# Optimization experiments

Hardware: AMD Instinct MI355X
Metric: run time of the kernel (lower is better)

## Reference

```python
import jax, jax.numpy as jnp
import numpy as np
import math

H = 16
SEG = 128
DIL = 2


def hilbert_perm(M: int) -> jnp.ndarray:
    # Boustrophedon (snake) traversal of a ceil(sqrt(M)) grid, matching
    # create_hilbert_mapping_simple: skip linear positions >= M, keep first M.
    g = int(math.ceil(math.sqrt(M)))
    grid = np.arange(g * g).reshape(g, g)
    grid[1::2] = grid[1::2, ::-1]
    flat = grid.reshape(-1)
    flat = flat[flat < M][:M]
    return jnp.asarray(flat, dtype=jnp.int32)


def setup_inputs() -> dict:
    key = jax.random.key(0)
    kx, kq, ko = jax.random.split(key, 3)
    B, M, D = 4, 4096, 1024
    x = jax.random.normal(kx, (B, M, D), dtype=jnp.float32)
    # nn.Linear weights: [out_features, in_features], y = x @ W.T
    w_qkv = jax.random.normal(kq, (3 * D, D), dtype=jnp.float32) * (D ** -0.5)
    w_out = jax.random.normal(ko, (D, D), dtype=jnp.float32) * (D ** -0.5)
    return {"x": x, "w_qkv": w_qkv, "w_out": w_out}


def reference(x, w_qkv, w_out):
    B, M, Dm = x.shape
    hd = Dm // H
    scale = hd ** -0.5
    S = M // SEG  # number of segments (M chosen as a multiple of SEG)

    qkv = x @ w_qkv.T                              # [B, M, 3*Dm]
    qkv = qkv.reshape(B, M, 3, H, hd)
    q = qkv[:, :, 0].transpose(0, 2, 1, 3)         # [B, H, M, hd]
    k = qkv[:, :, 1].transpose(0, 2, 1, 3)
    v = qkv[:, :, 2].transpose(0, 2, 1, 3)

    perm = hilbert_perm(M)
    qh = q[:, :, perm]                             # Hilbert-reordered
    kh = k[:, :, perm]
    vh = v[:, :, perm]

    # segment-local dilated attention: each query attends to keys at
    # positions seg_start + j*DIL within its own segment
    qh = qh.reshape(B, H, S, SEG, hd)
    kd = kh.reshape(B, H, S, SEG, hd)[:, :, :, ::DIL]   # [B,H,S,SEG//DIL,hd]
    vd = vh.reshape(B, H, S, SEG, hd)[:, :, :, ::DIL]

    scores = jnp.einsum('bhsqd,bhskd->bhsqk', qh * scale, kd)
    attn = jax.nn.softmax(scores, axis=-1)
    o = jnp.einsum('bhsqk,bhskd->bhsqd', attn, vd)       # [B,H,S,SEG,hd]
    o = o.reshape(B, H, M, hd).transpose(0, 2, 1, 3).reshape(B, M, Dm)
    return o @ w_out.T
```

## Files before the change

### kernel.cpp

```cpp
#include <hip/hip_runtime.h>


typedef _Float16 f16x8 __attribute__((ext_vector_type(8)));
typedef _Float16 f16x4 __attribute__((ext_vector_type(4)));
typedef float f32x4 __attribute__((ext_vector_type(4)));

__device__ __forceinline__ int hperm(int i) {
  int r = i >> 6, c = i & 63;
  return (r << 6) | ((r & 1) ? (63 - c) : c);
}

__device__ __forceinline__ int arow_gather(int mp) {
  int b = mp >> 11, i = mp & 2047;
  int s = i >> 6, j = i & 63;
  return b * 4096 + hperm(s * 128 + 2 * j);
}

__device__ __forceinline__ void gload_lds16(const _Float16* g, _Float16* l) {
  __builtin_amdgcn_global_load_lds(
      (const __attribute__((address_space(1))) void*)g,
      (__attribute__((address_space(3))) void*)l, 16, 0, 0);
}

__global__ __launch_bounds__(256) void cast_f32_f16(
    const float* __restrict__ s, _Float16* __restrict__ d, int n4) {
  int i = blockIdx.x * 256 + threadIdx.x;
  if (i >= n4) return;
  float4 v = ((const float4*)s)[i];
  f16x4 o;
  o[0] = (_Float16)v.x;
  o[1] = (_Float16)v.y;
  o[2] = (_Float16)v.z;
  o[3] = (_Float16)v.w;
  *(f16x4*)&d[(size_t)i * 4] = o;
}


#define BAR __builtin_amdgcn_s_barrier()
#define LGKM0                                          \
  do {                                                 \
    asm volatile("s_waitcnt lgkmcnt(0)" ::: "memory"); \
    __builtin_amdgcn_sched_barrier(0);                 \
  } while (0)
#define VM4 asm volatile("s_waitcnt vmcnt(4)" ::: "memory")

#define STG(mat, kt, h, buf)                                          \
  do {                                                                \
    if ((kt) < NK) {                                                  \
      const _Float16* g0 = ((mat) ? gpB : gpA)[(h)*2] + (size_t)(kt)*64;   \
      const _Float16* g1 = ((mat) ? gpB : gpA)[(h)*2 + 1] + (size_t)(kt)*64; \
      _Float16* d_ = &lds[buf][mat][h][t * 8];                        \
      gload_lds16(g0, d_);                                            \
      gload_lds16(g1, d_ + 4096);                                     \
    }                                                                 \
  } while (0)

#define LDA_(buf, mh)                                            \
  _Pragma("unroll") for (int m = 0; m < 4; m++) {                \
    a[0][m] = *(const f16x8*)(aB[buf][0] + (mh)*4096 + m * 1024); \
    a[1][m] = *(const f16x8*)(aB[buf][1] + (mh)*4096 + m * 1024); \
  }

#define LDB_(buf, nh)                                                      \
  _Pragma("unroll") for (int nf = 0; nf < 2; nf++) {                       \
    b[nh][0][nf] = *(const f16x8*)(bB[buf][0] + (nh)*2048 + nf * 1024);    \
    b[nh][1][nf] = *(const f16x8*)(bB[buf][1] + (nh)*2048 + nf * 1024);    \
  }

#define MM_(mh, nh)                                                        \
  __builtin_amdgcn_s_setprio(1);                                           \
  _Pragma("unroll") for (int m = 0; m < 4; m++)                            \
      _Pragma("unroll") for (int nf = 0; nf < 2; nf++)                     \
          _Pragma("unroll") for (int ks = 0; ks < 2; ks++) acc[(mh)*4 + m] \
              [(nh)*2 + nf] = __builtin_amdgcn_mfma_f32_16x16x32_f16(      \
                  a[ks][m], b[nh][ks][nf], acc[(mh)*4 + m][(nh)*2 + nf],   \
                  0, 0, 0);                                                \
  __builtin_amdgcn_s_setprio(0);

template <typename OutT, bool GATHER>
__global__ __launch_bounds__(512, 2) void gemm_nt_8ph(
    const _Float16* __restrict__ A, const _Float16* __restrict__ B,
    OutT* __restrict__ C, int N, int K, int NB) {
  __shared__ _Float16 lds[2][2][2][8192];
  const int t = threadIdx.x;
  const int lane = t & 63, wave = t >> 6;
  const int wm = wave >> 2, wn = wave & 3;
  const int lr = lane & 15, lg = lane >> 4;

  const int nwg = gridDim.x;
  const int id = blockIdx.x;
  const int sw = (id & 7) * (nwg >> 3) + (id >> 3);
  const int bn = sw % NB, bm = sw / NB;

  const size_t arow0 = (size_t)bm * 256;
  const size_t brow0 = (size_t)bn * 256;
  const int NK = K >> 6;

  const int sgrow = t >> 3;
  const int sgcol = ((t & 7) * 8) ^ ((sgrow & 7) << 3);
  const _Float16* gpA[4];
  const _Float16* gpB[4];
#pragma unroll
  for (int r = 0; r < 4; r++) {
    int mr = bm * 256 + 64 * r + sgrow;
    int ar = GATHER ? arow_gather(mr) : mr;
    gpA[r] = A + (size_t)ar * K + sgcol;
    gpB[r] = B + (brow0 + 64 * r + sgrow) * (size_t)K + sgcol;
  }

  const int cx0 = (lg * 8) ^ ((lr & 7) << 3);
  const int cx1 = cx0 ^ 32;
  const _Float16* aB[2][2];
  const _Float16* bB[2][2];
#pragma unroll
  for (int bf = 0; bf < 2; bf++) {
    aB[bf][0] = &lds[bf][0][wm][lr * 64 + cx0];
    aB[bf][1] = &lds[bf][0][wm][lr * 64 + cx1];
    bB[bf][0] = &lds[bf][1][wn >> 1][(wn & 1) * 4096 + lr * 64 + cx0];
    bB[bf][1] = &lds[bf][1][wn >> 1][(wn & 1) * 4096 + lr * 64 + cx1];
  }

  f32x4 acc[8][4] = {};
  f16x8 a[2][4], b[2][2][2];

  STG(0, 0, 0, 0);
  STG(0, 0, 1, 0);
  STG(1, 0, 0, 0);
  STG(1, 0, 1, 0);
  STG(1, 1, 0, 1);
  STG(1, 1, 1, 1);
  VM4;
  BAR;

  for (int i = 0; i < NK / 2; i++) {
    const int k1 = 2 * i + 1, k2 = 2 * i + 2, k3 = 2 * i + 3;
    LDA_(0, 0); LDB_(0, 0); STG(0, k1, 0, 1); BAR; LGKM0; MM_(0, 0); BAR;
    LDB_(0, 1);             STG(0, k1, 1, 1); BAR; LGKM0; MM_(0, 1); BAR;
    LDA_(0, 1);             STG(1, k2, 0, 0); BAR; LGKM0; MM_(1, 1); BAR;
                            STG(1, k2, 1, 0); VM4; BAR; LGKM0; MM_(1, 0); BAR;
    LDA_(1, 0); LDB_(1, 0); STG(0, k2, 0, 0); BAR; LGKM0; MM_(0, 0); BAR;
    LDB_(1, 1);             STG(0, k2, 1, 0); BAR; LGKM0; MM_(0, 1); BAR;
    LDA_(1, 1);             STG(1, k3, 0, 1); BAR; LGKM0; MM_(1, 1); BAR;
                            STG(1, k3, 1, 1); VM4; BAR; LGKM0; MM_(1, 0); BAR;
  }

#pragma unroll
  for (int mf = 0; mf < 8; mf++) {
    size_t row0 = arow0 + wm * 128 + mf * 16 + lg * 4;
#pragma unroll
    for (int nf = 0; nf < 4; nf++) {
      size_t col = brow0 + wn * 64 + nf * 16 + lr;
#pragma unroll
      for (int j = 0; j < 4; j++)
        C[(row0 + j) * N + col] = (OutT)acc[mf][nf][j];
    }
  }
}

#define STRD 72

__global__ __launch_bounds__(256) void hilbert_attn(
    const _Float16* __restrict__ qh, const _Float16* __restrict__ kvh,
    _Float16* __restrict__ aout) {
  __shared__ _Float16 Qs[128 * STRD];
  __shared__ _Float16 Ks[64 * STRD];
  __shared__ _Float16 Vt[64 * STRD];
  __shared__ _Float16 Ps[128 * STRD];
  const int blk = blockIdx.x;
  const int s = blk & 31, h = (blk >> 5) & 15, b = blk >> 9;
  const int t = threadIdx.x, lane = t & 63, wave = t >> 6;
  const int lr = lane & 15, lg = lane >> 4, lk = lg * 8;
  const int col = (t & 7) * 8, rr = t >> 3;
  const size_t kvb = ((size_t)b * 2048 + s * 64) * 2048;

#pragma unroll
  for (int i = 0; i < 4; i++) {
    int m = i * 32 + rr;
    int p = b * 4096 + hperm(s * 128 + m);
    *(f16x8*)&Qs[m * STRD + col] =
        *(const f16x8*)&qh[(size_t)p * 1024 + h * 64 + col];
  }
#pragma unroll
  for (int i = 0; i < 2; i++) {
    int j = i * 32 + rr;
    *(f16x8*)&Ks[j * STRD + col] =
        *(const f16x8*)&kvh[kvb + (size_t)j * 2048 + h * 64 + col];
    f16x8 vv =
        *(const f16x8*)&kvh[kvb + (size_t)j * 2048 + 1024 + h * 64 + col];
#pragma unroll
    for (int e = 0; e < 8; e++) Vt[(col + e) * STRD + j] = vv[e];
  }
  __syncthreads();

  f32x4 accs[2][4] = {};
#pragma unroll
  for (int kk = 0; kk < 2; kk++) {
    f16x8 aa[2], bb[4];
#pragma unroll
    for (int m = 0; m < 2; m++)
      aa[m] = *(const f16x8*)&Qs[(wave * 32 + m * 16 + lr) * STRD + kk * 32 + lk];
#pragma unroll
    for (int n = 0; n < 4; n++)
      bb[n] = *(const f16x8*)&Ks[(n * 16 + lr) * STRD + kk * 32 + lk];
#pragma unroll
    for (int m = 0; m < 2; m++)
#pragma unroll
      for (int n = 0; n < 4; n++)
        accs[m][n] =
            __builtin_amdgcn_mfma_f32_16x16x32_f16(aa[m], bb[n], accs[m][n], 0, 0, 0);
  }

#pragma unroll
  for (int m = 0; m < 2; m++) {
#pragma unroll
    for (int j = 0; j < 4; j++) {
      float sc0 = accs[m][0][j] * 0.125f;
      float sc1 = accs[m][1][j] * 0.125f;
      float sc2 = accs[m][2][j] * 0.125f;
      float sc3 = accs[m][3][j] * 0.125f;
      float mx = fmaxf(fmaxf(sc0, sc1), fmaxf(sc2, sc3));
#pragma unroll
      for (int d = 1; d < 16; d <<= 1) mx = fmaxf(mx, __shfl_xor(mx, d, 16));
      float e0 = __expf(sc0 - mx), e1 = __expf(sc1 - mx);
      float e2 = __expf(sc2 - mx), e3 = __expf(sc3 - mx);
      float sum = (e0 + e1) + (e2 + e3);
#pragma unroll
      for (int d = 1; d < 16; d <<= 1) sum += __shfl_xor(sum, d, 16);
      float inv = 1.0f / sum;
      int row = wave * 32 + m * 16 + lg * 4 + j;
      Ps[row * STRD + 0 * 16 + lr] = (_Float16)(e0 * inv);
      Ps[row * STRD + 1 * 16 + lr] = (_Float16)(e1 * inv);
      Ps[row * STRD + 2 * 16 + lr] = (_Float16)(e2 * inv);
      Ps[row * STRD + 3 * 16 + lr] = (_Float16)(e3 * inv);
    }
  }
  __syncthreads();

  f32x4 acco[2][4] = {};
#pragma unroll
  for (int kk = 0; kk < 2; kk++) {
    f16x8 aa[2], bb[4];
#pragma unroll
    for (int m = 0; m < 2; m++)
      aa[m] = *(const f16x8*)&Ps[(wave * 32 + m * 16 + lr) * STRD + kk * 32 + lk];
#pragma unroll
    for (int n = 0; n < 4; n++)
      bb[n] = *(const f16x8*)&Vt[(n * 16 + lr) * STRD + kk * 32 + lk];
#pragma unroll
    for (int m = 0; m < 2; m++)
#pragma unroll
      for (int n = 0; n < 4; n++)
        acco[m][n] =
            __builtin_amdgcn_mfma_f32_16x16x32_f16(aa[m], bb[n], acco[m][n], 0, 0, 0);
  }

  const size_t orow0 = (size_t)b * 4096 + s * 128;
#pragma unroll
  for (int m = 0; m < 2; m++) {
#pragma unroll
    for (int n = 0; n < 4; n++) {
#pragma unroll
      for (int j = 0; j < 4; j++) {
        size_t row = orow0 + wave * 32 + m * 16 + lg * 4 + j;
        aout[row * 1024 + h * 64 + n * 16 + lr] = (_Float16)acco[m][n][j];
      }
    }
  }
}

extern "C" void kernel_launch(void* const* d_in, const int* in_sizes, int n_in,
                              void* d_out, int out_size, void* d_ws, size_t ws_size,
                              hipStream_t stream) {
  const float* x = (const float*)d_in[0];
  const float* w_qkv = (const float*)d_in[1];
  const float* w_out = (const float*)d_in[2];
  float* out = (float*)d_out;
  char* ws = (char*)d_ws;

  _Float16* xh = (_Float16*)(ws + 0);
  _Float16* wqh = (_Float16*)(ws + (size_t)33554432);
  _Float16* woh = (_Float16*)(ws + (size_t)39845888);
  _Float16* qh = (_Float16*)(ws + (size_t)41943040);
  _Float16* kvh = (_Float16*)(ws + (size_t)75497472);
  _Float16* atth = (_Float16*)(ws + (size_t)109051904);

  cast_f32_f16<<<16384, 256, 0, stream>>>(x, xh, 4194304);
  cast_f32_f16<<<3072, 256, 0, stream>>>(w_qkv, wqh, 786432);
  cast_f32_f16<<<1024, 256, 0, stream>>>(w_out, woh, 262144);

  gemm_nt_8ph<_Float16, false><<<256, 512, 0, stream>>>(xh, wqh, qh,
                                                        1024, 1024, 4);
  gemm_nt_8ph<_Float16, true><<<256, 512, 0, stream>>>(
      xh, wqh + (size_t)1024 * 1024, kvh, 2048, 1024, 8);
  hilbert_attn<<<2048, 256, 0, stream>>>(qh, kvh, atth);
  gemm_nt_8ph<float, false><<<256, 512, 0, stream>>>(atth, woh, out,
                                                     1024, 1024, 4);
}
```

Baseline: 173.1 us.

## Fuse cast launches and Q/KV GEMMs, peel last K-iteration, add early LDS wait

Merges the three f32-to-f16 cast kernels into one launch and the Q and KV projection GEMMs into a single 512-block grid, so there are fewer kernel launches and the two GEMMs fill the GPU together. The GEMM main loop is specialised to K=1024 with a peeled final iteration, which removes the per-stage bounds checks and ends with a vmcnt(0) drain. An extra lgkmcnt(8) wait is placed before the first barrier of each phase. Hardcoding the sizes ties the kernel to these shapes, and the combined grid mixes the gathered and non-gathered A loads in one launch.

```diff
diff --git a/kernel.cpp b/kernel.cpp
--- a/kernel.cpp
+++ b/kernel.cpp
@@ -22,17 +22,28 @@
       (__attribute__((address_space(3))) void*)l, 16, 0, 0);
 }
 
-__global__ __launch_bounds__(256) void cast_f32_f16(
-    const float* __restrict__ s, _Float16* __restrict__ d, int n4) {
+__global__ __launch_bounds__(256) void cast_all(
+    const float* __restrict__ x, _Float16* __restrict__ xh,
+    const float* __restrict__ wq, _Float16* __restrict__ wqh,
+    const float* __restrict__ wo, _Float16* __restrict__ woh) {
   int i = blockIdx.x * 256 + threadIdx.x;
-  if (i >= n4) return;
-  float4 v = ((const float4*)s)[i];
+  const float* s;
+  _Float16* d;
+  int j;
+  if (i < 4194304) {
+    s = x; d = xh; j = i;
+  } else if (i < 4194304 + 786432) {
+    s = wq; d = wqh; j = i - 4194304;
+  } else {
+    s = wo; d = woh; j = i - (4194304 + 786432);
+  }
+  float4 v = ((const float4*)s)[j];
   f16x4 o;
   o[0] = (_Float16)v.x;
   o[1] = (_Float16)v.y;
   o[2] = (_Float16)v.z;
   o[3] = (_Float16)v.w;
-  *(f16x4*)&d[(size_t)i * 4] = o;
+  *(f16x4*)&d[(size_t)j * 4] = o;
 }
 
 
@@ -42,17 +53,17 @@
     asm volatile("s_waitcnt lgkmcnt(0)" ::: "memory"); \
     __builtin_amdgcn_sched_barrier(0);                 \
   } while (0)
+#define LGKM8 asm volatile("s_waitcnt lgkmcnt(8)" ::: "memory")
 #define VM4 asm volatile("s_waitcnt vmcnt(4)" ::: "memory")
-
-#define STG(mat, kt, h, buf)                                          \
-  do {                                                                \
-    if ((kt) < NK) {                                                  \
-      const _Float16* g0 = ((mat) ? gpB : gpA)[(h)*2] + (size_t)(kt)*64;   \
-      const _Float16* g1 = ((mat) ? gpB : gpA)[(h)*2 + 1] + (size_t)(kt)*64; \
-      _Float16* d_ = &lds[buf][mat][h][t * 8];                        \
-      gload_lds16(g0, d_);                                            \
-      gload_lds16(g1, d_ + 4096);                                     \
-    }                                                                 \
+#define VM0 asm volatile("s_waitcnt vmcnt(0)" ::: "memory")
+
+#define STG(mat, kt, h, buf)                                                 \
+  do {                                                                       \
+    const _Float16* g0 = ((mat) ? gpB : gpA)[(h)*2] + (size_t)(kt)*64;       \
+    const _Float16* g1 = ((mat) ? gpB : gpA)[(h)*2 + 1] + (size_t)(kt)*64;   \
+    _Float16* d_ = &lds[buf][mat][h][t * 8];                                 \
+    gload_lds16(g0, d_);                                                     \
+    gload_lds16(g1, d_ + 4096);                                              \
   } while (0)
 
 #define LDA_(buf, mh)                                            \
@@ -61,10 +72,10 @@
     a[1][m] = *(const f16x8*)(aB[buf][1] + (mh)*4096 + m * 1024); \
   }
 
-#define LDB_(buf, nh)                                                      \
-  _Pragma("unroll") for (int nf = 0; nf < 2; nf++) {                       \
-    b[nh][0][nf] = *(const f16x8*)(bB[buf][0] + (nh)*2048 + nf * 1024);    \
-    b[nh][1][nf] = *(const f16x8*)(bB[buf][1] + (nh)*2048 + nf * 1024);    \
+#define LDB_(buf, nh)                                                   \
+  _Pragma("unroll") for (int nf = 0; nf < 2; nf++) {                    \
+    b[nh][0][nf] = *(const f16x8*)(bB[buf][0] + (nh)*2048 + nf * 1024); \
+    b[nh][1][nf] = *(const f16x8*)(bB[buf][1] + (nh)*2048 + nf * 1024); \
   }
 
 #define MM_(mh, nh)                                                        \
@@ -77,36 +88,15 @@
                   0, 0, 0);                                                \
   __builtin_amdgcn_s_setprio(0);
 
-template <typename OutT, bool GATHER>
-__global__ __launch_bounds__(512, 2) void gemm_nt_8ph(
-    const _Float16* __restrict__ A, const _Float16* __restrict__ B,
-    OutT* __restrict__ C, int N, int K, int NB) {
-  __shared__ _Float16 lds[2][2][2][8192];
+template <typename OutT>
+__device__ __forceinline__ void gemm_body(
+    const _Float16* const* gpA, const _Float16* const* gpB,
+    OutT* __restrict__ C, int N, size_t arow0, size_t brow0,
+    _Float16 (&lds)[2][2][2][8192]) {
   const int t = threadIdx.x;
   const int lane = t & 63, wave = t >> 6;
   const int wm = wave >> 2, wn = wave & 3;
   const int lr = lane & 15, lg = lane >> 4;
-
-  const int nwg = gridDim.x;
-  const int id = blockIdx.x;
-  const int sw = (id & 7) * (nwg >> 3) + (id >> 3);
-  const int bn = sw % NB, bm = sw / NB;
-
-  const size_t arow0 = (size_t)bm * 256;
-  const size_t brow0 = (size_t)bn * 256;
-  const int NK = K >> 6;
-
-  const int sgrow = t >> 3;
-  const int sgcol = ((t & 7) * 8) ^ ((sgrow & 7) << 3);
-  const _Float16* gpA[4];
-  const _Float16* gpB[4];
-#pragma unroll
-  for (int r = 0; r < 4; r++) {
-    int mr = bm * 256 + 64 * r + sgrow;
-    int ar = GATHER ? arow_gather(mr) : mr;
-    gpA[r] = A + (size_t)ar * K + sgcol;
-    gpB[r] = B + (brow0 + 64 * r + sgrow) * (size_t)K + sgcol;
-  }
 
   const int cx0 = (lg * 8) ^ ((lr & 7) << 3);
   const int cx1 = cx0 ^ 32;
@@ -132,16 +122,27 @@
   VM4;
   BAR;
 
-  for (int i = 0; i < NK / 2; i++) {
+  for (int i = 0; i < 7; i++) {
     const int k1 = 2 * i + 1, k2 = 2 * i + 2, k3 = 2 * i + 3;
-    LDA_(0, 0); LDB_(0, 0); STG(0, k1, 0, 1); BAR; LGKM0; MM_(0, 0); BAR;
-    LDB_(0, 1);             STG(0, k1, 1, 1); BAR; LGKM0; MM_(0, 1); BAR;
-    LDA_(0, 1);             STG(1, k2, 0, 0); BAR; LGKM0; MM_(1, 1); BAR;
-                            STG(1, k2, 1, 0); VM4; BAR; LGKM0; MM_(1, 0); BAR;
-    LDA_(1, 0); LDB_(1, 0); STG(0, k2, 0, 0); BAR; LGKM0; MM_(0, 0); BAR;
-    LDB_(1, 1);             STG(0, k2, 1, 0); BAR; LGKM0; MM_(0, 1); BAR;
-    LDA_(1, 1);             STG(1, k3, 0, 1); BAR; LGKM0; MM_(1, 1); BAR;
-                            STG(1, k3, 1, 1); VM4; BAR; LGKM0; MM_(1, 0); BAR;
+    LDA_(0, 0); LDB_(0, 0); STG(0, k1, 0, 1); LGKM8; BAR; LGKM0; MM_(0, 0); BAR;
+    LDB_(0, 1);             STG(0, k1, 1, 1);        BAR; LGKM0; MM_(0, 1); BAR;
+    LDA_(0, 1);             STG(1, k2, 0, 0);        BAR; LGKM0; MM_(1, 1); BAR;
+                            STG(1, k2, 1, 0); VM4;   BAR; LGKM0; MM_(1, 0); BAR;
+    LDA_(1, 0); LDB_(1, 0); STG(0, k2, 0, 0); LGKM8; BAR; LGKM0; MM_(0, 0); BAR;
+    LDB_(1, 1);             STG(0, k2, 1, 0);        BAR; LGKM0; MM_(0, 1); BAR;
+    LDA_(1, 1);             STG(1, k3, 0, 1);        BAR; LGKM0; MM_(1, 1); BAR;
+                            STG(1, k3, 1, 1); VM4;   BAR; LGKM0; MM_(1, 0); BAR;
+  }
+
+  {
+    LDA_(0, 0); LDB_(0, 0); STG(0, 15, 0, 1); LGKM8; BAR; LGKM0; MM_(0, 0); BAR;
+    LDB_(0, 1);             STG(0, 15, 1, 1);        BAR; LGKM0; MM_(0, 1); BAR;
+    LDA_(0, 1);                                      BAR; LGKM0; MM_(1, 1); BAR;
+                                              VM0;   BAR; LGKM0; MM_(1, 0); BAR;
+    LDA_(1, 0); LDB_(1, 0);                          BAR; LGKM0; MM_(0, 0); BAR;
+    LDB_(1, 1);                                      BAR; LGKM0; MM_(0, 1); BAR;
+    LDA_(1, 1);                                      BAR; LGKM0; MM_(1, 1); BAR;
+                                                          LGKM0; MM_(1, 0);
   }
 
 #pragma unroll
@@ -155,6 +156,57 @@
         C[(row0 + j) * N + col] = (OutT)acc[mf][nf][j];
     }
   }
+}
+
+__global__ __launch_bounds__(512, 2) void gemm_qkv8(
+    const _Float16* __restrict__ xh, const _Float16* __restrict__ wqh,
+    _Float16* __restrict__ qh, _Float16* __restrict__ kvh) {
+  __shared__ _Float16 lds[2][2][2][8192];
+  const int t = threadIdx.x;
+  const int id = blockIdx.x;
+  const int sw = (id & 7) * (gridDim.x >> 3) + (id >> 3);
+  const bool iskv = sw >= 256;
+  const int wid = iskv ? sw - 256 : sw;
+  const int N = iskv ? 2048 : 1024;
+  const int bn = iskv ? (wid & 7) : (wid & 3);
+  const int bm = iskv ? (wid >> 3) : (wid >> 2);
+  const _Float16* Bw = wqh + (iskv ? (size_t)1048576 : 0);
+  _Float16* C = iskv ? kvh : qh;
+
+  const int sgrow = t >> 3;
+  const int sgcol = ((t & 7) * 8) ^ ((sgrow & 7) << 3);
+  const _Float16* gpA[4];
+  const _Float16* gpB[4];
+#pragma unroll
+  for (int r = 0; r < 4; r++) {
+    int mr = bm * 256 + 64 * r + sgrow;
+    int ar = iskv ? arow_gather(mr) : mr;
+    gpA[r] = xh + (size_t)ar * 1024 + sgcol;
+    gpB[r] = Bw + ((size_t)bn * 256 + 64 * r + sgrow) * 1024 + sgcol;
+  }
+  gemm_body<_Float16>(gpA, gpB, C, N, (size_t)bm * 256, (size_t)bn * 256, lds);
+}
+
+__global__ __launch_bounds__(512, 2) void gemm_out8(
+    const _Float16* __restrict__ atth, const _Float16* __restrict__ woh,
+    float* __restrict__ out) {
+  __shared__ _Float16 lds[2][2][2][8192];
+  const int t = threadIdx.x;
+  const int id = blockIdx.x;
+  const int sw = (id & 7) * (gridDim.x >> 3) + (id >> 3);
+  const int bn = sw & 3, bm = sw >> 2;
+
+  const int sgrow = t >> 3;
+  const int sgcol = ((t & 7) * 8) ^ ((sgrow & 7) << 3);
+  const _Float16* gpA[4];
+  const _Float16* gpB[4];
+#pragma unroll
+  for (int r = 0; r < 4; r++) {
+    gpA[r] = atth + ((size_t)bm * 256 + 64 * r + sgrow) * 1024 + sgcol;
+    gpB[r] = woh + ((size_t)bn * 256 + 64 * r + sgrow) * 1024 + sgcol;
+  }
+  gemm_body<float>(gpA, gpB, out, 1024, (size_t)bm * 256, (size_t)bn * 256,
+                   lds);
 }
 
 #define STRD 72
@@ -284,15 +336,9 @@
   _Float16* kvh = (_Float16*)(ws + (size_t)75497472);
   _Float16* atth = (_Float16*)(ws + (size_t)109051904);
 
-  cast_f32_f16<<<16384, 256, 0, stream>>>(x, xh, 4194304);
-  cast_f32_f16<<<3072, 256, 0, stream>>>(w_qkv, wqh, 786432);
-  cast_f32_f16<<<1024, 256, 0, stream>>>(w_out, woh, 262144);
-
-  gemm_nt_8ph<_Float16, false><<<256, 512, 0, stream>>>(xh, wqh, qh,
-                                                        1024, 1024, 4);
-  gemm_nt_8ph<_Float16, true><<<256, 512, 0, stream>>>(
-      xh, wqh + (size_t)1024 * 1024, kvh, 2048, 1024, 8);
+  cast_all<<<20480, 256, 0, stream>>>(x, xh, w_qkv, wqh, w_out, woh);
+
+  gemm_qkv8<<<512, 512, 0, stream>>>(xh, wqh, qh, kvh);
   hilbert_attn<<<2048, 256, 0, stream>>>(qh, kvh, atth);
-  gemm_nt_8ph<float, false><<<256, 512, 0, stream>>>(atth, woh, out,
-                                                     1024, 1024, 4);
-}
+  gemm_out8<<<256, 512, 0, stream>>>(atth, woh, out);
+}
```

New measurement: 161.2 us. 6.9% less time.
